# Performance work log

Hardware: AMD Instinct MI355X
Metric: run time of the kernel (lower is better)

The kernel has to match this reference:

```python
import jax, jax.numpy as jnp
import numpy as np

WINDOW_SIZE = 512
NUM_HEADS = 16
HIDDEN = 1024
HEAD_DIM = HIDDEN // NUM_HEADS
SCALING = HEAD_DIM ** (-0.5)


def sliding_window_mask(seq_len, window_size):
    # row i attends to cols j with i - w//2 <= j <= i + w//2 (clipped to bounds)
    i = jnp.arange(seq_len)[:, None]
    j = jnp.arange(seq_len)[None, :]
    half = window_size // 2
    return jnp.abs(i - j) <= half  # [S, S] bool


def setup_inputs() -> dict:
    key = jax.random.key(0)
    k0, k1, k2, k3, k4 = jax.random.split(key, 5)
    B, S = 2, 2048
    hidden_states = jax.random.normal(k0, (B, S, HIDDEN), dtype=jnp.float32)
    scale = 0.02
    Wq = jax.random.normal(k1, (HIDDEN, HIDDEN), dtype=jnp.float32) * scale
    Wk = jax.random.normal(k2, (HIDDEN, HIDDEN), dtype=jnp.float32) * scale
    Wv = jax.random.normal(k3, (HIDDEN, HIDDEN), dtype=jnp.float32) * scale
    Wo = jax.random.normal(k4, (HIDDEN, HIDDEN), dtype=jnp.float32) * scale
    return {"hidden_states": hidden_states, "Wq": Wq, "Wk": Wk, "Wv": Wv, "Wo": Wo}


def reference(hidden_states, Wq, Wk, Wv, Wo):
    B, S, _ = hidden_states.shape
    # nn.Linear(bias=False): y = x @ W.T
    def proj(x, W):
        y = jnp.einsum('bsh,oh->bso', x, W)
        return y.reshape(B, S, NUM_HEADS, HEAD_DIM).transpose(0, 2, 1, 3)  # [B,H,S,D]

    q = proj(hidden_states, Wq)
    k = proj(hidden_states, Wk)
    v = proj(hidden_states, Wv)

    mask = sliding_window_mask(S, WINDOW_SIZE)  # [S,S]
    scores = jnp.einsum('bhsd,bhtd->bhst', q, k) * SCALING  # [B,H,S,S]
    scores = jnp.where(mask[None, None], scores, -jnp.inf)
    attn = jax.nn.softmax(scores, axis=-1)
    out = jnp.einsum('bhst,bhtd->bhsd', attn, v)
    out = out.transpose(0, 2, 1, 3).reshape(B, S, HIDDEN)
    out = jnp.einsum('bsh,oh->bso', out, Wo)
    return out, attn
```

## Files before the change

kernel.cpp:

```cpp
#include <hip/hip_runtime.h>

typedef unsigned short u16;
typedef __attribute__((ext_vector_type(8))) __bf16 bf16x8;
typedef __attribute__((ext_vector_type(4))) float f32x4;

#define DEV __device__ __forceinline__
#define SEQ 2048

DEV void async16(void* lds, const void* gptr) {
  __builtin_amdgcn_global_load_lds(
      (const __attribute__((address_space(1))) unsigned int*)gptr,
      (__attribute__((address_space(3))) unsigned int*)lds, 16, 0, 0);
}

DEV u16 f2bf(float x) {
  unsigned u = __float_as_uint(x);
  return (u16)((u + 0x7fffu + ((u >> 16) & 1u)) >> 16);
}

DEV f32x4 mfma(bf16x8 a, bf16x8 b, f32x4 c) {
  return __builtin_amdgcn_mfma_f32_16x16x32_bf16(a, b, c, 0, 0, 0);
}

__global__ __launch_bounds__(256) void k_cvt(const float* __restrict__ src,
                                             u16* __restrict__ dst, int n) {
  int i = (blockIdx.x * 256 + threadIdx.x) * 4;
  if (i >= n) return;
  float4 v = *(const float4*)(src + i);
  ushort4 o = make_ushort4(f2bf(v.x), f2bf(v.y), f2bf(v.z), f2bf(v.w));
  *(ushort4*)(dst + i) = o;
}

DEV void gemm_mainloop(const u16* __restrict__ A, const u16* __restrict__ B,
                       int K, u16* As, u16* Bs, f32x4 (&acc)[4][4], int tid) {
  const int wid = tid >> 6, lane = tid & 63;
  const int wm = wid >> 1, wn = wid & 1;
  const int quad = lane >> 4, l15 = lane & 15;
  const int ci0 = tid, ci1 = tid + 256;
  const int r0 = ci0 >> 2, g0 = (ci0 & 3) ^ (r0 & 3);
  const int r1 = ci1 >> 2, g1 = (ci1 & 3) ^ (r1 & 3);
  u16* ldsA0 = As + wid * 512;
  u16* ldsA1 = As + wid * 512 + 2048;
  u16* ldsB0 = Bs + wid * 512;
  u16* ldsB1 = Bs + wid * 512 + 2048;

  for (int k0 = 0; k0 < K; k0 += 32) {
    __syncthreads();
    async16(ldsA0, A + (size_t)r0 * K + k0 + g0 * 8);
    async16(ldsA1, A + (size_t)r1 * K + k0 + g1 * 8);
    async16(ldsB0, B + (size_t)r0 * K + k0 + g0 * 8);
    async16(ldsB1, B + (size_t)r1 * K + k0 + g1 * 8);
    __syncthreads();
    bf16x8 af[4], bf[4];
#pragma unroll
    for (int mt = 0; mt < 4; ++mt) {
      int row = wm * 64 + mt * 16 + l15;
      af[mt] = *(const bf16x8*)(As + row * 32 + (quad ^ (row & 3)) * 8);
    }
#pragma unroll
    for (int nt = 0; nt < 4; ++nt) {
      int row = wn * 64 + nt * 16 + l15;
      bf[nt] = *(const bf16x8*)(Bs + row * 32 + (quad ^ (row & 3)) * 8);
    }
#pragma unroll
    for (int mt = 0; mt < 4; ++mt)
#pragma unroll
      for (int nt = 0; nt < 4; ++nt)
        acc[mt][nt] = mfma(af[mt], bf[nt], acc[mt][nt]);
  }
}

__global__ __launch_bounds__(256) void k_gemm_qkv(
    const u16* __restrict__ X, const u16* __restrict__ Wq,
    const u16* __restrict__ Wk, const u16* __restrict__ Wv,
    u16* __restrict__ Q16, u16* __restrict__ K16, u16* __restrict__ Vt16) {
  __shared__ u16 As[128 * 32], Bs[128 * 32];
  const int tid = threadIdx.x;
  const int bm = blockIdx.x, bn = blockIdx.y, z = blockIdx.z;
  const u16* B = (z == 0) ? Wq : (z == 1) ? Wk : Wv;
  f32x4 acc[4][4];
#pragma unroll
  for (int i = 0; i < 4; ++i)
#pragma unroll
    for (int j = 0; j < 4; ++j) acc[i][j] = (f32x4){0.f, 0.f, 0.f, 0.f};
  gemm_mainloop(X + (size_t)bm * 128 * 1024, B + (size_t)bn * 128 * 1024, 1024,
                As, Bs, acc, tid);
  const int wid = tid >> 6, lane = tid & 63;
  const int wm = wid >> 1, wn = wid & 1, quad = lane >> 4, l15 = lane & 15;
#pragma unroll
  for (int mt = 0; mt < 4; ++mt)
#pragma unroll
    for (int nt = 0; nt < 4; ++nt)
#pragma unroll
      for (int r = 0; r < 4; ++r) {
        int row = bm * 128 + wm * 64 + mt * 16 + quad * 4 + r;
        int col = bn * 128 + wn * 64 + nt * 16 + l15;
        int b = row >> 11, s = row & 2047, h = col >> 6, d = col & 63;
        int bh = b * 16 + h;
        u16 v = f2bf(acc[mt][nt][r]);
        if (z == 2)
          Vt16[((size_t)bh * 64 + d) * SEQ + s] = v;
        else {
          u16* dst = (z == 0) ? Q16 : K16;
          dst[((size_t)bh * SEQ + s) * 64 + d] = v;
        }
      }
}

__global__ __launch_bounds__(256) void k_gemm_out(const u16* __restrict__ A,
                                                  const u16* __restrict__ Bw,
                                                  float* __restrict__ out) {
  __shared__ u16 As[128 * 32], Bs[128 * 32];
  const int tid = threadIdx.x;
  f32x4 acc[4][4];
#pragma unroll
  for (int i = 0; i < 4; ++i)
#pragma unroll
    for (int j = 0; j < 4; ++j) acc[i][j] = (f32x4){0.f, 0.f, 0.f, 0.f};
  gemm_mainloop(A + (size_t)blockIdx.x * 128 * 1024,
                Bw + (size_t)blockIdx.y * 128 * 1024, 1024, As, Bs, acc, tid);
  const int wid = tid >> 6, lane = tid & 63;
  const int wm = wid >> 1, wn = wid & 1, quad = lane >> 4, l15 = lane & 15;
#pragma unroll
  for (int mt = 0; mt < 4; ++mt)
#pragma unroll
    for (int nt = 0; nt < 4; ++nt)
#pragma unroll
      for (int r = 0; r < 4; ++r) {
        int row = blockIdx.x * 128 + wm * 64 + mt * 16 + quad * 4 + r;
        int col = blockIdx.y * 128 + wn * 64 + nt * 16 + l15;
        out[(size_t)row * 1024 + col] = acc[mt][nt][r];
      }
}

__global__ __launch_bounds__(256) void k_attn(
    const u16* __restrict__ Q16, const u16* __restrict__ K16,
    const u16* __restrict__ Vt16, float* __restrict__ attn_out,
    u16* __restrict__ O16) {
  __shared__ u16 Qt[64 * 64];
  __shared__ u16 Kt[64 * 64];
  __shared__ u16 Vt[64 * 64];
  __shared__ u16 P[64 * 72];
  __shared__ float rowsum[64];

  const int tid = threadIdx.x, wid = tid >> 6, lane = tid & 63;
  const int quad = lane >> 4, l15 = lane & 15;
  const int qbase = blockIdx.x * 64;
  const int bh = blockIdx.y;
  const int b = bh >> 4, h = bh & 15;
  const u16* Qb = Q16 + ((size_t)bh * SEQ + qbase) * 64;
  const u16* Kb = K16 + (size_t)bh * SEQ * 64;
  const u16* Vb = Vt16 + (size_t)bh * 64 * SEQ;
  float* attn_b = attn_out + (size_t)bh * SEQ * SEQ;

  const int ci0 = tid, ci1 = tid + 256;
  const int r0 = ci0 >> 3, g0 = (ci0 & 7) ^ (r0 & 7);
  const int r1 = ci1 >> 3, g1 = (ci1 & 7) ^ (r1 & 7);

  async16(Qt + wid * 512, Qb + r0 * 64 + g0 * 8);
  async16(Qt + wid * 512 + 2048, Qb + r1 * 64 + g1 * 8);
  if (tid < 64) rowsum[tid] = 0.f;
  __syncthreads();
  bf16x8 aq[4][2];
#pragma unroll
  for (int mt = 0; mt < 4; ++mt)
#pragma unroll
    for (int ks = 0; ks < 2; ++ks) {
      int row = mt * 16 + l15;
      aq[mt][ks] =
          *(const bf16x8*)(Qt + row * 64 + (((ks * 4 + quad) ^ (row & 7)) * 8));
    }

  float racc[4][4];
#pragma unroll
  for (int mt = 0; mt < 4; ++mt)
#pragma unroll
    for (int r = 0; r < 4; ++r) racc[mt][r] = 0.f;

  for (int t = 0; t < 9; ++t) {
    int jbase = qbase - 256 + t * 64;
    if (jbase < 0 || jbase > SEQ - 64) continue;
    __syncthreads();
    async16(Kt + wid * 512, Kb + (size_t)(jbase + r0) * 64 + g0 * 8);
    async16(Kt + wid * 512 + 2048, Kb + (size_t)(jbase + r1) * 64 + g1 * 8);
    __syncthreads();
    bf16x8 bq[2];
#pragma unroll
    for (int ks = 0; ks < 2; ++ks) {
      int row = wid * 16 + l15;
      bq[ks] =
          *(const bf16x8*)(Kt + row * 64 + (((ks * 4 + quad) ^ (row & 7)) * 8));
    }
    int j = jbase + wid * 16 + l15;
#pragma unroll
    for (int mt = 0; mt < 4; ++mt) {
      f32x4 c = (f32x4){0.f, 0.f, 0.f, 0.f};
      c = mfma(aq[mt][0], bq[0], c);
      c = mfma(aq[mt][1], bq[1], c);
#pragma unroll
      for (int r = 0; r < 4; ++r) {
        int i_ = qbase + mt * 16 + quad * 4 + r;
        int dlt = i_ - j;
        dlt = dlt < 0 ? -dlt : dlt;
        if (dlt <= 256) racc[mt][r] += __expf(c[r] * 0.125f);
      }
    }
  }
#pragma unroll
  for (int mt = 0; mt < 4; ++mt)
#pragma unroll
    for (int r = 0; r < 4; ++r) {
      float v = racc[mt][r];
      v += __shfl_xor(v, 1, 16);
      v += __shfl_xor(v, 2, 16);
      v += __shfl_xor(v, 4, 16);
      v += __shfl_xor(v, 8, 16);
      racc[mt][r] = v;
    }
  if (l15 == 0) {
#pragma unroll
    for (int mt = 0; mt < 4; ++mt)
#pragma unroll
      for (int r = 0; r < 4; ++r)
        atomicAdd(&rowsum[mt * 16 + quad * 4 + r], racc[mt][r]);
  }
  __syncthreads();
  float linv[4][4];
#pragma unroll
  for (int mt = 0; mt < 4; ++mt)
#pragma unroll
    for (int r = 0; r < 4; ++r)
      linv[mt][r] = 1.0f / rowsum[mt * 16 + quad * 4 + r];

  f32x4 oacc[4];
#pragma unroll
  for (int mt = 0; mt < 4; ++mt) oacc[mt] = (f32x4){0.f, 0.f, 0.f, 0.f};

  for (int t = 0; t < 9; ++t) {
    int jbase = qbase - 256 + t * 64;
    if (jbase < 0 || jbase > SEQ - 64) continue;
    __syncthreads();
    async16(Kt + wid * 512, Kb + (size_t)(jbase + r0) * 64 + g0 * 8);
    async16(Kt + wid * 512 + 2048, Kb + (size_t)(jbase + r1) * 64 + g1 * 8);
    async16(Vt + wid * 512, Vb + (size_t)r0 * SEQ + jbase + g0 * 8);
    async16(Vt + wid * 512 + 2048, Vb + (size_t)r1 * SEQ + jbase + g1 * 8);
    __syncthreads();
    bf16x8 bq[2], bv[2];
#pragma unroll
    for (int ks = 0; ks < 2; ++ks) {
      int row = wid * 16 + l15;
      int sw = ((ks * 4 + quad) ^ (row & 7)) * 8;
      bq[ks] = *(const bf16x8*)(Kt + row * 64 + sw);
      bv[ks] = *(const bf16x8*)(Vt + row * 64 + sw);
    }
    int j = jbase + wid * 16 + l15;
#pragma unroll
    for (int mt = 0; mt < 4; ++mt) {
      f32x4 c = (f32x4){0.f, 0.f, 0.f, 0.f};
      c = mfma(aq[mt][0], bq[0], c);
      c = mfma(aq[mt][1], bq[1], c);
#pragma unroll
      for (int r = 0; r < 4; ++r) {
        int i_ = qbase + mt * 16 + quad * 4 + r;
        int dlt = i_ - j;
        dlt = dlt < 0 ? -dlt : dlt;
        float a = 0.f;
        if (dlt <= 256) a = __expf(c[r] * 0.125f) * linv[mt][r];
        attn_b[(size_t)i_ * SEQ + j] = a;
        P[(mt * 16 + quad * 4 + r) * 72 + wid * 16 + l15] = f2bf(a);
      }
    }
    __syncthreads();
#pragma unroll
    for (int mt = 0; mt < 4; ++mt) {
      int row = mt * 16 + l15;
      bf16x8 ap0 = *(const bf16x8*)(P + row * 72 + quad * 8);
      bf16x8 ap1 = *(const bf16x8*)(P + row * 72 + 32 + quad * 8);
      oacc[mt] = mfma(ap0, bv[0], oacc[mt]);
      oacc[mt] = mfma(ap1, bv[1], oacc[mt]);
    }
  }
#pragma unroll
  for (int mt = 0; mt < 4; ++mt)
#pragma unroll
    for (int r = 0; r < 4; ++r) {
      int i_ = qbase + mt * 16 + quad * 4 + r;
      int d = wid * 16 + l15;
      O16[((size_t)b * SEQ + i_) * 1024 + h * 64 + d] = f2bf(oacc[mt][r]);
    }
}

extern "C" void kernel_launch(void* const* d_in, const int* in_sizes, int n_in,
                              void* d_out, int out_size, void* d_ws,
                              size_t ws_size, hipStream_t stream) {
  const float* hs = (const float*)d_in[0];
  const float* Wq = (const float*)d_in[1];
  const float* Wk = (const float*)d_in[2];
  const float* Wv = (const float*)d_in[3];
  const float* Wo = (const float*)d_in[4];
  float* out = (float*)d_out;
  float* attn = out + (size_t)4194304;

  u16* X16 = (u16*)d_ws;
  u16* Wq16 = X16 + 4194304;
  u16* Wk16 = Wq16 + 1048576;
  u16* Wv16 = Wk16 + 1048576;
  u16* Wo16 = Wv16 + 1048576;
  u16* Q16 = Wo16 + 1048576;
  u16* K16 = Q16 + 4194304;
  u16* Vt16 = K16 + 4194304;
  u16* O16 = Vt16 + 4194304;

  k_cvt<<<4096, 256, 0, stream>>>(hs, X16, 4194304);
  k_cvt<<<1024, 256, 0, stream>>>(Wq, Wq16, 1048576);
  k_cvt<<<1024, 256, 0, stream>>>(Wk, Wk16, 1048576);
  k_cvt<<<1024, 256, 0, stream>>>(Wv, Wv16, 1048576);
  k_cvt<<<1024, 256, 0, stream>>>(Wo, Wo16, 1048576);

  k_gemm_qkv<<<dim3(32, 8, 3), 256, 0, stream>>>(X16, Wq16, Wk16, Wv16, Q16,
                                                 K16, Vt16);
  k_attn<<<dim3(32, 32), 256, 0, stream>>>(Q16, K16, Vt16, attn, O16);
  k_gemm_out<<<dim3(32, 8), 256, 0, stream>>>(O16, Wo16, out);
}
```

Baseline: 623.2 us.

## Single-pass attention: stash exp values, defer normalization, coalesced attn writes

The attention kernel now computes QK^T and exp only once. The unnormalized bf16 probabilities are stashed in registers and multiplied against V in that same pass, and the output is rescaled by the row-sum inverse at the end. The attn matrix is then written in a second phase, staged through an LDS float tile so each row goes out as coalesced nontemporal 16-byte stores. V is stored untransposed, which makes the QKV GEMM epilogue uniform, and the five conversion launches are merged into one. The cost is heavy register use for the stash, a more complex swizzle, and bf16-rounded probabilities written into attn instead of fp32 values.

```diff
diff --git a/kernel.cpp b/kernel.cpp
--- a/kernel.cpp
+++ b/kernel.cpp
@@ -6,6 +6,7 @@
 
 #define DEV __device__ __forceinline__
 #define SEQ 2048
+#define SWZ(r) ((((r) & 7)) ^ (((r) >> 3) & 7))
 
 DEV void async16(void* lds, const void* gptr) {
   __builtin_amdgcn_global_load_lds(
@@ -22,13 +23,29 @@
   return __builtin_amdgcn_mfma_f32_16x16x32_bf16(a, b, c, 0, 0, 0);
 }
 
-__global__ __launch_bounds__(256) void k_cvt(const float* __restrict__ src,
-                                             u16* __restrict__ dst, int n) {
-  int i = (blockIdx.x * 256 + threadIdx.x) * 4;
-  if (i >= n) return;
+__global__ __launch_bounds__(256) void k_cvt_all(
+    const float* __restrict__ hs, const float* __restrict__ wq,
+    const float* __restrict__ wk, const float* __restrict__ wv,
+    const float* __restrict__ wo, u16* __restrict__ X16,
+    u16* __restrict__ W16) {
+  int b = blockIdx.x;
+  const float* src;
+  u16* dst;
+  int off;
+  if (b < 4096) {
+    src = hs;
+    dst = X16;
+    off = b * 1024;
+  } else {
+    int b2 = b - 4096;
+    int w = b2 >> 10;
+    src = (w == 0) ? wq : (w == 1) ? wk : (w == 2) ? wv : wo;
+    dst = W16 + (size_t)w * 1048576;
+    off = (b2 & 1023) * 1024;
+  }
+  int i = off + threadIdx.x * 4;
   float4 v = *(const float4*)(src + i);
-  ushort4 o = make_ushort4(f2bf(v.x), f2bf(v.y), f2bf(v.z), f2bf(v.w));
-  *(ushort4*)(dst + i) = o;
+  *(ushort4*)(dst + i) = make_ushort4(f2bf(v.x), f2bf(v.y), f2bf(v.z), f2bf(v.w));
 }
 
 DEV void gemm_mainloop(const u16* __restrict__ A, const u16* __restrict__ B,
@@ -73,11 +90,12 @@
 __global__ __launch_bounds__(256) void k_gemm_qkv(
     const u16* __restrict__ X, const u16* __restrict__ Wq,
     const u16* __restrict__ Wk, const u16* __restrict__ Wv,
-    u16* __restrict__ Q16, u16* __restrict__ K16, u16* __restrict__ Vt16) {
+    u16* __restrict__ Q16, u16* __restrict__ K16, u16* __restrict__ V16) {
   __shared__ u16 As[128 * 32], Bs[128 * 32];
   const int tid = threadIdx.x;
   const int bm = blockIdx.x, bn = blockIdx.y, z = blockIdx.z;
   const u16* B = (z == 0) ? Wq : (z == 1) ? Wk : Wv;
+  u16* dst = (z == 0) ? Q16 : (z == 1) ? K16 : V16;
   f32x4 acc[4][4];
 #pragma unroll
   for (int i = 0; i < 4; ++i)
@@ -97,13 +115,7 @@
         int col = bn * 128 + wn * 64 + nt * 16 + l15;
         int b = row >> 11, s = row & 2047, h = col >> 6, d = col & 63;
         int bh = b * 16 + h;
-        u16 v = f2bf(acc[mt][nt][r]);
-        if (z == 2)
-          Vt16[((size_t)bh * 64 + d) * SEQ + s] = v;
-        else {
-          u16* dst = (z == 0) ? Q16 : K16;
-          dst[((size_t)bh * SEQ + s) * 64 + d] = v;
-        }
+        dst[((size_t)bh * SEQ + s) * 64 + d] = f2bf(acc[mt][nt][r]);
       }
 }
 
@@ -133,14 +145,19 @@
       }
 }
 
-__global__ __launch_bounds__(256) void k_attn(
+__global__ __launch_bounds__(256, 2) void k_attn(
     const u16* __restrict__ Q16, const u16* __restrict__ K16,
-    const u16* __restrict__ Vt16, float* __restrict__ attn_out,
+    const u16* __restrict__ V16, float* __restrict__ attn_out,
     u16* __restrict__ O16) {
-  __shared__ u16 Qt[64 * 64];
-  __shared__ u16 Kt[64 * 64];
-  __shared__ u16 Vt[64 * 64];
-  __shared__ u16 P[64 * 72];
+  __shared__ union alignas(16) U {
+    struct {
+      u16 Qt[64 * 64];
+      u16 Kt[64 * 64];
+      u16 Vt[64 * 64];
+      u16 P[64 * 72];
+    } s;
+    float Pf[64 * 68];
+  } sm;
   __shared__ float rowsum[64];
 
   const int tid = threadIdx.x, wid = tid >> 6, lane = tid & 63;
@@ -150,62 +167,93 @@
   const int b = bh >> 4, h = bh & 15;
   const u16* Qb = Q16 + ((size_t)bh * SEQ + qbase) * 64;
   const u16* Kb = K16 + (size_t)bh * SEQ * 64;
-  const u16* Vb = Vt16 + (size_t)bh * 64 * SEQ;
+  const u16* Vb = V16 + (size_t)bh * SEQ * 64;
   float* attn_b = attn_out + (size_t)bh * SEQ * SEQ;
 
-  const int ci0 = tid, ci1 = tid + 256;
-  const int r0 = ci0 >> 3, g0 = (ci0 & 7) ^ (r0 & 7);
-  const int r1 = ci1 >> 3, g1 = (ci1 & 7) ^ (r1 & 7);
-
-  async16(Qt + wid * 512, Qb + r0 * 64 + g0 * 8);
-  async16(Qt + wid * 512 + 2048, Qb + r1 * 64 + g1 * 8);
+  const int r0 = tid >> 3, g0 = (tid & 7) ^ SWZ(r0);
+  const int r1 = r0 + 32, g1 = (tid & 7) ^ SWZ(r1);
+
+  async16(sm.s.Qt + wid * 512, Qb + r0 * 64 + g0 * 8);
+  async16(sm.s.Qt + wid * 512 + 2048, Qb + (size_t)r1 * 64 + g1 * 8);
   if (tid < 64) rowsum[tid] = 0.f;
-  __syncthreads();
-  bf16x8 aq[4][2];
-#pragma unroll
-  for (int mt = 0; mt < 4; ++mt)
-#pragma unroll
-    for (int ks = 0; ks < 2; ++ks) {
-      int row = mt * 16 + l15;
-      aq[mt][ks] =
-          *(const bf16x8*)(Qt + row * 64 + (((ks * 4 + quad) ^ (row & 7)) * 8));
-    }
 
   float racc[4][4];
-#pragma unroll
-  for (int mt = 0; mt < 4; ++mt)
+  f32x4 oacc[4];
+#pragma unroll
+  for (int mt = 0; mt < 4; ++mt) {
+    oacc[mt] = (f32x4){0.f, 0.f, 0.f, 0.f};
 #pragma unroll
     for (int r = 0; r < 4; ++r) racc[mt][r] = 0.f;
-
+  }
+  unsigned stash[9][8];
+  const int d = wid * 16 + l15;
+
+#pragma unroll
   for (int t = 0; t < 9; ++t) {
-    int jbase = qbase - 256 + t * 64;
+    const int jbase = qbase - 256 + t * 64;
     if (jbase < 0 || jbase > SEQ - 64) continue;
     __syncthreads();
-    async16(Kt + wid * 512, Kb + (size_t)(jbase + r0) * 64 + g0 * 8);
-    async16(Kt + wid * 512 + 2048, Kb + (size_t)(jbase + r1) * 64 + g1 * 8);
+    async16(sm.s.Kt + wid * 512, Kb + (size_t)(jbase + r0) * 64 + g0 * 8);
+    async16(sm.s.Kt + wid * 512 + 2048, Kb + (size_t)(jbase + r1) * 64 + g1 * 8);
+    async16(sm.s.Vt + wid * 512, Vb + (size_t)(jbase + r0) * 64 + g0 * 8);
+    async16(sm.s.Vt + wid * 512 + 2048, Vb + (size_t)(jbase + r1) * 64 + g1 * 8);
     __syncthreads();
     bf16x8 bq[2];
 #pragma unroll
     for (int ks = 0; ks < 2; ++ks) {
       int row = wid * 16 + l15;
-      bq[ks] =
-          *(const bf16x8*)(Kt + row * 64 + (((ks * 4 + quad) ^ (row & 7)) * 8));
-    }
-    int j = jbase + wid * 16 + l15;
+      bq[ks] = *(const bf16x8*)(sm.s.Kt + row * 64 +
+                                (((ks * 4 + quad) ^ SWZ(row)) * 8));
+    }
+    bf16x8 bv[2];
+#pragma unroll
+    for (int ks = 0; ks < 2; ++ks)
+#pragma unroll
+      for (int jj = 0; jj < 8; ++jj) {
+        int j = ks * 32 + quad * 8 + jj;
+        int slot = (d >> 3) ^ SWZ(j);
+        bv[ks][jj] = *(const __bf16*)(sm.s.Vt + j * 64 + slot * 8 + (d & 7));
+      }
+    const int jcol = jbase + wid * 16 + l15;
 #pragma unroll
     for (int mt = 0; mt < 4; ++mt) {
+      int arow = mt * 16 + l15;
+      bf16x8 a0 = *(const bf16x8*)(sm.s.Qt + arow * 64 + ((quad ^ SWZ(arow)) * 8));
+      bf16x8 a1 = *(const bf16x8*)(sm.s.Qt + arow * 64 +
+                                   (((4 + quad) ^ SWZ(arow)) * 8));
       f32x4 c = (f32x4){0.f, 0.f, 0.f, 0.f};
-      c = mfma(aq[mt][0], bq[0], c);
-      c = mfma(aq[mt][1], bq[1], c);
+      c = mfma(a0, bq[0], c);
+      c = mfma(a1, bq[1], c);
+      unsigned p0 = 0, p1 = 0;
 #pragma unroll
       for (int r = 0; r < 4; ++r) {
         int i_ = qbase + mt * 16 + quad * 4 + r;
-        int dlt = i_ - j;
+        int dlt = i_ - jcol;
         dlt = dlt < 0 ? -dlt : dlt;
-        if (dlt <= 256) racc[mt][r] += __expf(c[r] * 0.125f);
+        float e = 0.f;
+        if (dlt <= 256) e = __expf(c[r] * 0.125f);
+        racc[mt][r] += e;
+        unsigned eb = f2bf(e);
+        sm.s.P[(mt * 16 + quad * 4 + r) * 72 + wid * 16 + l15] = (u16)eb;
+        if (r == 0) p0 = eb;
+        if (r == 1) p0 |= eb << 16;
+        if (r == 2) p1 = eb;
+        if (r == 3) p1 |= eb << 16;
       }
-    }
-  }
+      stash[t][mt * 2] = p0;
+      stash[t][mt * 2 + 1] = p1;
+    }
+    __syncthreads();
+#pragma unroll
+    for (int mt = 0; mt < 4; ++mt) {
+      int row = mt * 16 + l15;
+      bf16x8 ap0 = *(const bf16x8*)(sm.s.P + row * 72 + quad * 8);
+      bf16x8 ap1 = *(const bf16x8*)(sm.s.P + row * 72 + 32 + quad * 8);
+      oacc[mt] = mfma(ap0, bv[0], oacc[mt]);
+      oacc[mt] = mfma(ap1, bv[1], oacc[mt]);
+    }
+  }
+
 #pragma unroll
   for (int mt = 0; mt < 4; ++mt)
 #pragma unroll
@@ -232,62 +280,42 @@
     for (int r = 0; r < 4; ++r)
       linv[mt][r] = 1.0f / rowsum[mt * 16 + quad * 4 + r];
 
-  f32x4 oacc[4];
-#pragma unroll
-  for (int mt = 0; mt < 4; ++mt) oacc[mt] = (f32x4){0.f, 0.f, 0.f, 0.f};
-
-  for (int t = 0; t < 9; ++t) {
-    int jbase = qbase - 256 + t * 64;
-    if (jbase < 0 || jbase > SEQ - 64) continue;
-    __syncthreads();
-    async16(Kt + wid * 512, Kb + (size_t)(jbase + r0) * 64 + g0 * 8);
-    async16(Kt + wid * 512 + 2048, Kb + (size_t)(jbase + r1) * 64 + g1 * 8);
-    async16(Vt + wid * 512, Vb + (size_t)r0 * SEQ + jbase + g0 * 8);
-    async16(Vt + wid * 512 + 2048, Vb + (size_t)r1 * SEQ + jbase + g1 * 8);
-    __syncthreads();
-    bf16x8 bq[2], bv[2];
-#pragma unroll
-    for (int ks = 0; ks < 2; ++ks) {
-      int row = wid * 16 + l15;
-      int sw = ((ks * 4 + quad) ^ (row & 7)) * 8;
-      bq[ks] = *(const bf16x8*)(Kt + row * 64 + sw);
-      bv[ks] = *(const bf16x8*)(Vt + row * 64 + sw);
-    }
-    int j = jbase + wid * 16 + l15;
-#pragma unroll
-    for (int mt = 0; mt < 4; ++mt) {
-      f32x4 c = (f32x4){0.f, 0.f, 0.f, 0.f};
-      c = mfma(aq[mt][0], bq[0], c);
-      c = mfma(aq[mt][1], bq[1], c);
-#pragma unroll
-      for (int r = 0; r < 4; ++r) {
-        int i_ = qbase + mt * 16 + quad * 4 + r;
-        int dlt = i_ - j;
-        dlt = dlt < 0 ? -dlt : dlt;
-        float a = 0.f;
-        if (dlt <= 256) a = __expf(c[r] * 0.125f) * linv[mt][r];
-        attn_b[(size_t)i_ * SEQ + j] = a;
-        P[(mt * 16 + quad * 4 + r) * 72 + wid * 16 + l15] = f2bf(a);
-      }
-    }
-    __syncthreads();
-#pragma unroll
-    for (int mt = 0; mt < 4; ++mt) {
-      int row = mt * 16 + l15;
-      bf16x8 ap0 = *(const bf16x8*)(P + row * 72 + quad * 8);
-      bf16x8 ap1 = *(const bf16x8*)(P + row * 72 + 32 + quad * 8);
-      oacc[mt] = mfma(ap0, bv[0], oacc[mt]);
-      oacc[mt] = mfma(ap1, bv[1], oacc[mt]);
-    }
-  }
 #pragma unroll
   for (int mt = 0; mt < 4; ++mt)
 #pragma unroll
     for (int r = 0; r < 4; ++r) {
       int i_ = qbase + mt * 16 + quad * 4 + r;
-      int d = wid * 16 + l15;
-      O16[((size_t)b * SEQ + i_) * 1024 + h * 64 + d] = f2bf(oacc[mt][r]);
-    }
+      O16[((size_t)b * SEQ + i_) * 1024 + h * 64 + d] =
+          f2bf(oacc[mt][r] * linv[mt][r]);
+    }
+
+  const int wcol = (tid & 15) * 4, wrow = tid >> 4;
+#pragma unroll
+  for (int t = 0; t < 9; ++t) {
+    const int jbase = qbase - 256 + t * 64;
+    if (jbase < 0 || jbase > SEQ - 64) continue;
+    __syncthreads();
+#pragma unroll
+    for (int mt = 0; mt < 4; ++mt) {
+      unsigned p0 = stash[t][mt * 2], p1 = stash[t][mt * 2 + 1];
+      int rb = mt * 16 + quad * 4;
+      int cc = wid * 16 + l15;
+      sm.Pf[(rb + 0) * 68 + cc] = __uint_as_float(p0 << 16) * linv[mt][0];
+      sm.Pf[(rb + 1) * 68 + cc] =
+          __uint_as_float(p0 & 0xffff0000u) * linv[mt][1];
+      sm.Pf[(rb + 2) * 68 + cc] = __uint_as_float(p1 << 16) * linv[mt][2];
+      sm.Pf[(rb + 3) * 68 + cc] =
+          __uint_as_float(p1 & 0xffff0000u) * linv[mt][3];
+    }
+    __syncthreads();
+#pragma unroll
+    for (int k = 0; k < 4; ++k) {
+      int row = wrow + k * 16;
+      f32x4 v = *(const f32x4*)(sm.Pf + row * 68 + wcol);
+      __builtin_nontemporal_store(
+          v, (f32x4*)(attn_b + (size_t)(qbase + row) * SEQ + jbase + wcol));
+    }
+  }
 }
 
 extern "C" void kernel_launch(void* const* d_in, const int* in_sizes, int n_in,
@@ -308,17 +336,12 @@
   u16* Wo16 = Wv16 + 1048576;
   u16* Q16 = Wo16 + 1048576;
   u16* K16 = Q16 + 4194304;
-  u16* Vt16 = K16 + 4194304;
-  u16* O16 = Vt16 + 4194304;
-
-  k_cvt<<<4096, 256, 0, stream>>>(hs, X16, 4194304);
-  k_cvt<<<1024, 256, 0, stream>>>(Wq, Wq16, 1048576);
-  k_cvt<<<1024, 256, 0, stream>>>(Wk, Wk16, 1048576);
-  k_cvt<<<1024, 256, 0, stream>>>(Wv, Wv16, 1048576);
-  k_cvt<<<1024, 256, 0, stream>>>(Wo, Wo16, 1048576);
-
+  u16* V16 = K16 + 4194304;
+  u16* O16 = V16 + 4194304;
+
+  k_cvt_all<<<8192, 256, 0, stream>>>(hs, Wq, Wk, Wv, Wo, X16, Wq16);
   k_gemm_qkv<<<dim3(32, 8, 3), 256, 0, stream>>>(X16, Wq16, Wk16, Wv16, Q16,
-                                                 K16, Vt16);
-  k_attn<<<dim3(32, 32), 256, 0, stream>>>(Q16, K16, Vt16, attn, O16);
+                                                 K16, V16);
+  k_attn<<<dim3(32, 32), 256, 0, stream>>>(Q16, K16, V16, attn, O16);
   k_gemm_out<<<dim3(32, 8), 256, 0, stream>>>(O16, Wo16, out);
 }
```

After: 587.0 us. 5.8% less time.
